# Optimization experiments

Hardware: AMD Instinct MI355X
Metric: run time of the kernel (lower is better)

Reference implementation:

```python
import jax, jax.numpy as jnp
import numpy as np


def setup_inputs() -> dict:
    key = jax.random.key(0)
    k1, k2, k3, k4, k5 = jax.random.split(key, 5)
    b, t_q, t_k = 4, 256, 1024
    qs, ms, n = 512, 512, 128
    return {
        "query": jax.random.normal(k1, (b, t_q, qs), dtype=jnp.float32),
        "keys": jax.random.normal(k2, (b, t_k, ms), dtype=jnp.float32),
        "Wq": jax.random.normal(k3, (qs, n), dtype=jnp.float32) * 0.05,
        "Wk": jax.random.normal(k4, (ms, n), dtype=jnp.float32) * 0.05,
        "linear_att": jax.random.normal(k5, (n,), dtype=jnp.float32) * 0.05,
    }


def reference(query, keys, Wq, Wk, linear_att):
    # projections: b t_q n and b t_k n
    att_query = jnp.einsum("bqd,dn->bqn", query, Wq)
    att_keys = jnp.einsum("bkd,dn->bkn", keys, Wk)
    # Bahdanau additive score: tanh(q + k) . v  -> b t_q t_k
    sum_qk = att_query[:, :, None, :] + att_keys[:, None, :, :]
    scores = jnp.einsum("bqkn,n->bqk", jnp.tanh(sum_qk), linear_att)
    weights = jax.nn.softmax(scores, axis=-1)
    context = jnp.einsum("bqk,bkd->bqd", weights, keys)
    return (context, weights)
```

## Files before the change

kernel.cpp:

```cpp
#include <hip/hip_runtime.h>

#define B 4
#define TQ 256
#define TK 1024
#define QS 512
#define NN 128

#define TANH_SCALE 2.8853900817779268f
#define LOG2E 1.4426950408889634f

__device__ __forceinline__ float fast_exp2(float x) {
#if __has_builtin(__builtin_amdgcn_exp2f)
    return __builtin_amdgcn_exp2f(x);
#else
    return exp2f(x);
#endif
}
__device__ __forceinline__ float fast_rcp(float x) {
#if __has_builtin(__builtin_amdgcn_rcpf)
    return __builtin_amdgcn_rcpf(x);
#else
    return 1.0f / x;
#endif
}

__global__ __launch_bounds__(256) void proj_kernel(
    const float* __restrict__ query, const float* __restrict__ keys,
    const float* __restrict__ Wq, const float* __restrict__ Wk,
    float* __restrict__ attq, float* __restrict__ attkT)
{
    __shared__ float As[32][36];
    __shared__ float Bs[32][132];

    const int tid = threadIdx.x;
    const int rb = blockIdx.x * 32;
    const bool isq = (rb < B * TQ);
    const float* A = isq ? (query + (size_t)rb * QS)
                         : (keys + (size_t)(rb - B * TQ) * QS);
    const float* W = isq ? Wq : Wk;

    const int n0 = (tid & 31) * 4;
    const int q0 = (tid >> 5) * 4;
    float acc[4][4] = {};

    for (int k0 = 0; k0 < QS; k0 += 32) {
        {
            const int r = tid >> 3, c = tid & 7;
            const float4 v = *(const float4*)(A + (size_t)r * QS + k0 + c * 4);
            As[c * 4 + 0][r] = v.x;
            As[c * 4 + 1][r] = v.y;
            As[c * 4 + 2][r] = v.z;
            As[c * 4 + 3][r] = v.w;
        }
        {
            const int n = (tid & 31) * 4, r0 = tid >> 5;
            #pragma unroll
            for (int j = 0; j < 4; ++j) {
                const int kk = r0 + j * 8;
                *(float4*)&Bs[kk][n] =
                    *(const float4*)(W + (size_t)(k0 + kk) * NN + n);
            }
        }
        __syncthreads();
        #pragma unroll
        for (int kk = 0; kk < 32; ++kk) {
            const float4 a = *(const float4*)&As[kk][q0];
            const float4 b = *(const float4*)&Bs[kk][n0];
            const float av[4] = {a.x, a.y, a.z, a.w};
            const float bv[4] = {b.x, b.y, b.z, b.w};
            #pragma unroll
            for (int i = 0; i < 4; ++i)
                #pragma unroll
                for (int j = 0; j < 4; ++j)
                    acc[i][j] = fmaf(av[i], bv[j], acc[i][j]);
        }
        __syncthreads();
    }

    if (isq) {
        float* out = attq + (size_t)rb * NN;
        #pragma unroll
        for (int i = 0; i < 4; ++i) {
            float4 o;
            o.x = acc[i][0] * TANH_SCALE;
            o.y = acc[i][1] * TANH_SCALE;
            o.z = acc[i][2] * TANH_SCALE;
            o.w = acc[i][3] * TANH_SCALE;
            *(float4*)(out + (size_t)(q0 + i) * NN + n0) = o;
        }
    } else {
        #pragma unroll
        for (int i = 0; i < 4; ++i) {
            float4 o;
            o.x = acc[i][0] * TANH_SCALE;
            o.y = acc[i][1] * TANH_SCALE;
            o.z = acc[i][2] * TANH_SCALE;
            o.w = acc[i][3] * TANH_SCALE;
            *(float4*)&Bs[q0 + i][n0] = o;
        }
        __syncthreads();
        const int rk = rb - B * TQ;
        const int bb = rk >> 10;
        const int kbase = rk & 1023;
        const int n = tid >> 1;
        const int kh = (tid & 1) * 16;
        float* o = attkT + (size_t)bb * NN * TK + (size_t)n * TK + kbase + kh;
        #pragma unroll
        for (int m4 = 0; m4 < 4; ++m4) {
            float4 t;
            t.x = Bs[kh + m4 * 4 + 0][n];
            t.y = Bs[kh + m4 * 4 + 1][n];
            t.z = Bs[kh + m4 * 4 + 2][n];
            t.w = Bs[kh + m4 * 4 + 3][n];
            *(float4*)(o + m4 * 4) = t;
        }
    }
}

__global__ __launch_bounds__(256) void score_softmax_kernel(
    const float* __restrict__ attq, const float* __restrict__ attkT,
    const float* __restrict__ vatt, float* __restrict__ wout,
    float4* __restrict__ ctxz)
{
    __shared__ float aqs[2][128];
    __shared__ float vsm[128];
    __shared__ float red[2][8];

    const int tid = threadIdx.x;
    const int b = blockIdx.x >> 7;
    const int q0 = (blockIdx.x & 127) * 2;

    ctxz[(size_t)blockIdx.x * 256 + tid] = make_float4(0.f, 0.f, 0.f, 0.f);

    if (tid < 128) {
        aqs[0][tid] = attq[((size_t)b * TQ + q0) * NN + tid];
        vsm[tid] = vatt[tid];
    } else {
        aqs[1][tid & 127] = attq[((size_t)b * TQ + q0 + 1) * NN + (tid & 127)];
    }
    __syncthreads();

    const float* kt = attkT + (size_t)b * NN * TK + (size_t)tid * 4;
    float s[2][4] = {};

    #pragma unroll 4
    for (int n = 0; n < 128; ++n) {
        const float4 a = *(const float4*)(kt + (size_t)n * TK);
        const float a0 = aqs[0][n], a1 = aqs[1][n], vv = vsm[n];
        const float av[4] = {a.x, a.y, a.z, a.w};
        #pragma unroll
        for (int r = 0; r < 4; ++r) {
            const float x0 = a0 + av[r];
            const float t0 = fmaf(-2.f, fast_rcp(1.f + fast_exp2(x0)), 1.f);
            s[0][r] = fmaf(vv, t0, s[0][r]);
            const float x1 = a1 + av[r];
            const float t1 = fmaf(-2.f, fast_rcp(1.f + fast_exp2(x1)), 1.f);
            s[1][r] = fmaf(vv, t1, s[1][r]);
        }
    }

    const int lane = tid & 63, wid = tid >> 6;
    #pragma unroll
    for (int qq = 0; qq < 2; ++qq) {
        float mm = fmaxf(fmaxf(s[qq][0], s[qq][1]), fmaxf(s[qq][2], s[qq][3]));
        #pragma unroll
        for (int off = 32; off > 0; off >>= 1)
            mm = fmaxf(mm, __shfl_xor(mm, off, 64));
        if (lane == 0) red[qq][wid] = mm;
    }
    __syncthreads();
    float m[2];
    m[0] = fmaxf(fmaxf(red[0][0], red[0][1]), fmaxf(red[0][2], red[0][3]));
    m[1] = fmaxf(fmaxf(red[1][0], red[1][1]), fmaxf(red[1][2], red[1][3]));

    float e[2][4];
    #pragma unroll
    for (int qq = 0; qq < 2; ++qq) {
        float ls = 0.f;
        #pragma unroll
        for (int i = 0; i < 4; ++i) {
            e[qq][i] = fast_exp2((s[qq][i] - m[qq]) * LOG2E);
            ls += e[qq][i];
        }
        #pragma unroll
        for (int off = 32; off > 0; off >>= 1)
            ls += __shfl_xor(ls, off, 64);
        if (lane == 0) red[qq][4 + wid] = ls;
    }
    __syncthreads();
    #pragma unroll
    for (int qq = 0; qq < 2; ++qq) {
        const float S = red[qq][4] + red[qq][5] + red[qq][6] + red[qq][7];
        const float inv = fast_rcp(S);
        float4 w4;
        w4.x = e[qq][0] * inv; w4.y = e[qq][1] * inv;
        w4.z = e[qq][2] * inv; w4.w = e[qq][3] * inv;
        *(float4*)(wout + ((size_t)b * TQ + q0 + qq) * TK + (size_t)tid * 4) = w4;
    }
}

__global__ __launch_bounds__(256) void context_kernel(
    const float* __restrict__ keys, const float* __restrict__ w,
    float* __restrict__ ctx)
{
    __shared__ float Wst[32][34];
    __shared__ float Ks[32][64];

    const int tid = threadIdx.x;
    const int bid = blockIdx.x;
    const int b = bid >> 7;
    const int rem = bid & 127;
    const int qt = rem >> 4;
    const int dt = (rem >> 1) & 7;
    const int ks = rem & 1;

    const float* wb = w + (size_t)b * TQ * TK + (size_t)qt * 32 * TK + ks * 512;
    const float* kb = keys + (size_t)b * TK * QS + (size_t)ks * 512 * QS + dt * 64;

    const int d0 = (tid & 15) * 4;
    const int q0 = (tid >> 4) * 2;
    float acc[2][4] = {};

    for (int k0 = 0; k0 < 512; k0 += 32) {
        {
            const int r = tid >> 3, c = tid & 7;
            const float4 v = *(const float4*)(wb + (size_t)r * TK + k0 + c * 4);
            Wst[c * 4 + 0][r] = v.x;
            Wst[c * 4 + 1][r] = v.y;
            Wst[c * 4 + 2][r] = v.z;
            Wst[c * 4 + 3][r] = v.w;
        }
        {
            const int c = tid & 15, r = tid >> 4;
            *(float4*)&Ks[r][c * 4] =
                *(const float4*)(kb + (size_t)(k0 + r) * QS + c * 4);
            *(float4*)&Ks[r + 16][c * 4] =
                *(const float4*)(kb + (size_t)(k0 + r + 16) * QS + c * 4);
        }
        __syncthreads();
        #pragma unroll
        for (int kk = 0; kk < 32; ++kk) {
            const float2 a = *(const float2*)&Wst[kk][q0];
            const float4 bb = *(const float4*)&Ks[kk][d0];
            acc[0][0] = fmaf(a.x, bb.x, acc[0][0]);
            acc[0][1] = fmaf(a.x, bb.y, acc[0][1]);
            acc[0][2] = fmaf(a.x, bb.z, acc[0][2]);
            acc[0][3] = fmaf(a.x, bb.w, acc[0][3]);
            acc[1][0] = fmaf(a.y, bb.x, acc[1][0]);
            acc[1][1] = fmaf(a.y, bb.y, acc[1][1]);
            acc[1][2] = fmaf(a.y, bb.z, acc[1][2]);
            acc[1][3] = fmaf(a.y, bb.w, acc[1][3]);
        }
        __syncthreads();
    }

    float* op = ctx + ((size_t)b * TQ + qt * 32 + q0) * QS + dt * 64 + d0;
    #pragma unroll
    for (int i = 0; i < 2; ++i)
        #pragma unroll
        for (int j = 0; j < 4; ++j)
            atomicAdd(op + (size_t)i * QS + j, acc[i][j]);
}

extern "C" void kernel_launch(void* const* d_in, const int* in_sizes, int n_in,
                              void* d_out, int out_size, void* d_ws, size_t ws_size,
                              hipStream_t stream) {
    const float* query = (const float*)d_in[0];
    const float* keys  = (const float*)d_in[1];
    const float* Wq    = (const float*)d_in[2];
    const float* Wk    = (const float*)d_in[3];
    const float* vatt  = (const float*)d_in[4];

    float* ctx = (float*)d_out;
    float* wts = ctx + (size_t)B * TQ * QS;

    float* attq  = (float*)d_ws;
    float* attkT = attq + (size_t)B * TQ * NN;

    hipLaunchKernelGGL(proj_kernel, dim3((B * TQ + B * TK) / 32), dim3(256), 0,
                       stream, query, keys, Wq, Wk, attq, attkT);
    hipLaunchKernelGGL(score_softmax_kernel, dim3(B * TQ / 2), dim3(256), 0,
                       stream, attq, attkT, vatt, wts, (float4*)ctx);
    hipLaunchKernelGGL(context_kernel, dim3(512), dim3(256), 0,
                       stream, keys, wts, ctx);
}
```

Baseline: 163.3 us.

## Replace context atomics with split-K partial buffers plus reduce, shrink projection tiles

The context GEMM now splits K four ways across twice as many blocks and writes plain float4 partial sums into a workspace buffer. A new reduce kernel adds the four partials, replacing the float atomicAdds and the zeroing of ctx inside the score kernel. The projection kernel uses 16-row tiles, doubling its grid to improve occupancy, and the score loop unroll goes from 4 to 8. The cost is an extra kernel launch and extra global traffic for the partial buffers, about 8 MB written and read back.

Measured after the change: 149.5 us. -8.4%, faster.

```diff
diff --git a/kernel.cpp b/kernel.cpp
--- a/kernel.cpp
+++ b/kernel.cpp
@@ -29,28 +29,26 @@
     const float* __restrict__ Wq, const float* __restrict__ Wk,
     float* __restrict__ attq, float* __restrict__ attkT)
 {
-    __shared__ float As[32][36];
+    __shared__ float As[32][18];
     __shared__ float Bs[32][132];
 
     const int tid = threadIdx.x;
-    const int rb = blockIdx.x * 32;
+    const int rb = blockIdx.x * 16;
     const bool isq = (rb < B * TQ);
     const float* A = isq ? (query + (size_t)rb * QS)
                          : (keys + (size_t)(rb - B * TQ) * QS);
     const float* W = isq ? Wq : Wk;
 
     const int n0 = (tid & 31) * 4;
-    const int q0 = (tid >> 5) * 4;
-    float acc[4][4] = {};
+    const int q0 = (tid >> 5) * 2;
+    float acc[2][4] = {};
 
     for (int k0 = 0; k0 < QS; k0 += 32) {
         {
-            const int r = tid >> 3, c = tid & 7;
-            const float4 v = *(const float4*)(A + (size_t)r * QS + k0 + c * 4);
-            As[c * 4 + 0][r] = v.x;
-            As[c * 4 + 1][r] = v.y;
-            As[c * 4 + 2][r] = v.z;
-            As[c * 4 + 3][r] = v.w;
+            const int r = tid >> 4, c = tid & 15;
+            const float2 v = *(const float2*)(A + (size_t)r * QS + k0 + c * 2);
+            As[c * 2 + 0][r] = v.x;
+            As[c * 2 + 1][r] = v.y;
         }
         {
             const int n = (tid & 31) * 4, r0 = tid >> 5;
@@ -64,15 +62,16 @@
         __syncthreads();
         #pragma unroll
         for (int kk = 0; kk < 32; ++kk) {
-            const float4 a = *(const float4*)&As[kk][q0];
+            const float2 a = *(const float2*)&As[kk][q0];
             const float4 b = *(const float4*)&Bs[kk][n0];
-            const float av[4] = {a.x, a.y, a.z, a.w};
-            const float bv[4] = {b.x, b.y, b.z, b.w};
-            #pragma unroll
-            for (int i = 0; i < 4; ++i)
-                #pragma unroll
-                for (int j = 0; j < 4; ++j)
-                    acc[i][j] = fmaf(av[i], bv[j], acc[i][j]);
+            acc[0][0] = fmaf(a.x, b.x, acc[0][0]);
+            acc[0][1] = fmaf(a.x, b.y, acc[0][1]);
+            acc[0][2] = fmaf(a.x, b.z, acc[0][2]);
+            acc[0][3] = fmaf(a.x, b.w, acc[0][3]);
+            acc[1][0] = fmaf(a.y, b.x, acc[1][0]);
+            acc[1][1] = fmaf(a.y, b.y, acc[1][1]);
+            acc[1][2] = fmaf(a.y, b.z, acc[1][2]);
+            acc[1][3] = fmaf(a.y, b.w, acc[1][3]);
         }
         __syncthreads();
     }
@@ -80,7 +79,7 @@
     if (isq) {
         float* out = attq + (size_t)rb * NN;
         #pragma unroll
-        for (int i = 0; i < 4; ++i) {
+        for (int i = 0; i < 2; ++i) {
             float4 o;
             o.x = acc[i][0] * TANH_SCALE;
             o.y = acc[i][1] * TANH_SCALE;
@@ -90,7 +89,7 @@
         }
     } else {
         #pragma unroll
-        for (int i = 0; i < 4; ++i) {
+        for (int i = 0; i < 2; ++i) {
             float4 o;
             o.x = acc[i][0] * TANH_SCALE;
             o.y = acc[i][1] * TANH_SCALE;
@@ -103,10 +102,10 @@
         const int bb = rk >> 10;
         const int kbase = rk & 1023;
         const int n = tid >> 1;
-        const int kh = (tid & 1) * 16;
+        const int kh = (tid & 1) * 8;
         float* o = attkT + (size_t)bb * NN * TK + (size_t)n * TK + kbase + kh;
         #pragma unroll
-        for (int m4 = 0; m4 < 4; ++m4) {
+        for (int m4 = 0; m4 < 2; ++m4) {
             float4 t;
             t.x = Bs[kh + m4 * 4 + 0][n];
             t.y = Bs[kh + m4 * 4 + 1][n];
@@ -119,8 +118,7 @@
 
 __global__ __launch_bounds__(256) void score_softmax_kernel(
     const float* __restrict__ attq, const float* __restrict__ attkT,
-    const float* __restrict__ vatt, float* __restrict__ wout,
-    float4* __restrict__ ctxz)
+    const float* __restrict__ vatt, float* __restrict__ wout)
 {
     __shared__ float aqs[2][128];
     __shared__ float vsm[128];
@@ -129,8 +127,6 @@
     const int tid = threadIdx.x;
     const int b = blockIdx.x >> 7;
     const int q0 = (blockIdx.x & 127) * 2;
-
-    ctxz[(size_t)blockIdx.x * 256 + tid] = make_float4(0.f, 0.f, 0.f, 0.f);
 
     if (tid < 128) {
         aqs[0][tid] = attq[((size_t)b * TQ + q0) * NN + tid];
@@ -143,7 +139,7 @@
     const float* kt = attkT + (size_t)b * NN * TK + (size_t)tid * 4;
     float s[2][4] = {};
 
-    #pragma unroll 4
+    #pragma unroll 8
     for (int n = 0; n < 128; ++n) {
         const float4 a = *(const float4*)(kt + (size_t)n * TK);
         const float a0 = aqs[0][n], a1 = aqs[1][n], vv = vsm[n];
@@ -199,29 +195,31 @@
     }
 }
 
+#define CTX_ELEMS ((size_t)B * TQ * QS)
+
 __global__ __launch_bounds__(256) void context_kernel(
     const float* __restrict__ keys, const float* __restrict__ w,
-    float* __restrict__ ctx)
+    float* __restrict__ ctxp)
 {
     __shared__ float Wst[32][34];
     __shared__ float Ks[32][64];
 
     const int tid = threadIdx.x;
     const int bid = blockIdx.x;
-    const int b = bid >> 7;
-    const int rem = bid & 127;
-    const int qt = rem >> 4;
-    const int dt = (rem >> 1) & 7;
-    const int ks = rem & 1;
-
-    const float* wb = w + (size_t)b * TQ * TK + (size_t)qt * 32 * TK + ks * 512;
-    const float* kb = keys + (size_t)b * TK * QS + (size_t)ks * 512 * QS + dt * 64;
+    const int b = bid >> 8;
+    const int rem = bid & 255;
+    const int qt = rem >> 5;
+    const int dt = (rem >> 2) & 7;
+    const int ks = rem & 3;
+
+    const float* wb = w + (size_t)b * TQ * TK + (size_t)qt * 32 * TK + ks * 256;
+    const float* kb = keys + (size_t)b * TK * QS + (size_t)ks * 256 * QS + dt * 64;
 
     const int d0 = (tid & 15) * 4;
     const int q0 = (tid >> 4) * 2;
     float acc[2][4] = {};
 
-    for (int k0 = 0; k0 < 512; k0 += 32) {
+    for (int k0 = 0; k0 < 256; k0 += 32) {
         {
             const int r = tid >> 3, c = tid & 7;
             const float4 v = *(const float4*)(wb + (size_t)r * TK + k0 + c * 4);
@@ -254,12 +252,31 @@
         __syncthreads();
     }
 
-    float* op = ctx + ((size_t)b * TQ + qt * 32 + q0) * QS + dt * 64 + d0;
+    float* op = ctxp + (size_t)ks * CTX_ELEMS
+              + ((size_t)b * TQ + qt * 32 + q0) * QS + dt * 64 + d0;
     #pragma unroll
-    for (int i = 0; i < 2; ++i)
-        #pragma unroll
-        for (int j = 0; j < 4; ++j)
-            atomicAdd(op + (size_t)i * QS + j, acc[i][j]);
+    for (int i = 0; i < 2; ++i) {
+        float4 o;
+        o.x = acc[i][0]; o.y = acc[i][1]; o.z = acc[i][2]; o.w = acc[i][3];
+        *(float4*)(op + (size_t)i * QS) = o;
+    }
+}
+
+__global__ __launch_bounds__(256) void reduce_kernel(
+    const float4* __restrict__ ctxp, float4* __restrict__ ctx)
+{
+    const size_t idx = (size_t)blockIdx.x * 256 + threadIdx.x;
+    const size_t stride = CTX_ELEMS / 4;
+    const float4 a = ctxp[idx];
+    const float4 b = ctxp[idx + stride];
+    const float4 c = ctxp[idx + 2 * stride];
+    const float4 d = ctxp[idx + 3 * stride];
+    float4 o;
+    o.x = (a.x + b.x) + (c.x + d.x);
+    o.y = (a.y + b.y) + (c.y + d.y);
+    o.z = (a.z + b.z) + (c.z + d.z);
+    o.w = (a.w + b.w) + (c.w + d.w);
+    ctx[idx] = o;
 }
 
 extern "C" void kernel_launch(void* const* d_in, const int* in_sizes, int n_in,
@@ -272,15 +289,18 @@
     const float* vatt  = (const float*)d_in[4];
 
     float* ctx = (float*)d_out;
-    float* wts = ctx + (size_t)B * TQ * QS;
+    float* wts = ctx + CTX_ELEMS;
 
     float* attq  = (float*)d_ws;
     float* attkT = attq + (size_t)B * TQ * NN;
-
-    hipLaunchKernelGGL(proj_kernel, dim3((B * TQ + B * TK) / 32), dim3(256), 0,
+    float* ctxp  = attkT + (size_t)B * NN * TK;
+
+    hipLaunchKernelGGL(proj_kernel, dim3((B * TQ + B * TK) / 16), dim3(256), 0,
                        stream, query, keys, Wq, Wk, attq, attkT);
     hipLaunchKernelGGL(score_softmax_kernel, dim3(B * TQ / 2), dim3(256), 0,
-                       stream, attq, attkT, vatt, wts, (float4*)ctx);
-    hipLaunchKernelGGL(context_kernel, dim3(512), dim3(256), 0,
-                       stream, keys, wts, ctx);
-}
+                       stream, attq, attkT, vatt, wts);
+    hipLaunchKernelGGL(context_kernel, dim3(1024), dim3(256), 0,
+                       stream, keys, wts, ctxp);
+    hipLaunchKernelGGL(reduce_kernel, dim3((unsigned)(CTX_ELEMS / 4 / 256)), dim3(256), 0,
+                       stream, (const float4*)ctxp, (float4*)ctx);
+}
```
